# Performance work log

Hardware: AMD Instinct MI355X
Metric: run time of the kernel (lower is better)

The kernel has to match this reference:

```python
import jax, jax.numpy as jnp
import numpy as np

B, C, D, H, W = 2, 32, 96, 96, 96
RED = 16
INV_SQRT2 = 0.7071067811865476  # 1/sqrt(2), Haar analysis filter coefficient
BN_EPS = 1e-5


def _haar1(x, axis):
    # pywt 'haar' DWT on even-length signals: a[i]=(x[2i]+x[2i+1])/sqrt2, d[i]=(x[2i]-x[2i+1])/sqrt2
    e = jax.lax.slice_in_dim(x, 0, None, stride=2, axis=axis)
    o = jax.lax.slice_in_dim(x, 1, None, stride=2, axis=axis)
    return (e + o) * INV_SQRT2, (e - o) * INV_SQRT2


def haar_dwt3d(x):
    # x: (B, C, D, H, W). Separable 3D Haar DWT; key letters follow pywt dwtn
    # axis order (D, H, W): 'aad' = approx along D, approx along H, detail along W.
    aD, dD = _haar1(x, 2)
    aa, ad = _haar1(aD, 3)
    da, dd = _haar1(dD, 3)
    aaa, aad = _haar1(aa, 4)
    ada, add = _haar1(ad, 4)
    daa, dad = _haar1(da, 4)
    dda, ddd = _haar1(dd, 4)
    # per-channel grouping of 7 detail bands, then flatten to (B, 7C, D/2, H/2, W/2)
    high = jnp.stack([aad, ada, add, daa, dad, dda, ddd], axis=2)
    b, c = x.shape[0], x.shape[1]
    high = high.reshape(b, c * 7, *aaa.shape[2:])
    return aaa, high


def chan_attn(x, w1, w2):
    # AdaptiveAvgPool3d(1) -> FC(no bias) -> ReLU -> FC(no bias) -> Sigmoid -> scale
    y = x.mean(axis=(2, 3, 4))                     # (B, Ch)
    y = jax.nn.sigmoid(jnp.maximum(y @ w1.T, 0.0) @ w2.T)
    return x * y[:, :, None, None, None]


def setup_inputs() -> dict:
    key = jax.random.key(0)
    ks = jax.random.split(key, 7)
    x = jax.random.normal(ks[0], (B, C, D, H, W), dtype=jnp.float32)
    w1_low = jax.random.normal(ks[1], (C // RED, C), dtype=jnp.float32) * 0.1
    w2_low = jax.random.normal(ks[2], (C, C // RED), dtype=jnp.float32) * 0.1
    w1_high = jax.random.normal(ks[3], (7 * C // RED, 7 * C), dtype=jnp.float32) * 0.05
    w2_high = jax.random.normal(ks[4], (7 * C, 7 * C // RED), dtype=jnp.float32) * 0.05
    w_fuse = jax.random.normal(ks[5], (C, 8 * C), dtype=jnp.float32) * 0.05  # 1x1x1 conv kernel
    b_fuse = jnp.zeros((C,), dtype=jnp.float32)
    gamma = jnp.ones((C,), dtype=jnp.float32)
    beta = jnp.zeros((C,), dtype=jnp.float32)
    return dict(x=x, w1_low=w1_low, w2_low=w2_low, w1_high=w1_high, w2_high=w2_high,
                w_fuse=w_fuse, b_fuse=b_fuse, gamma=gamma, beta=beta)


def reference(x, w1_low, w2_low, w1_high, w2_high, w_fuse, b_fuse, gamma, beta):
    low, high = haar_dwt3d(x)                                  # (B,C,48,48,48), (B,7C,48,48,48)
    low = chan_attn(low, w1_low, w2_low)
    high = chan_attn(high, w1_high, w2_high)
    z = jnp.concatenate([low, high], axis=1)                   # (B, 8C, 48,48,48)
    z = jnp.einsum('bcdhw,oc->bodhw', z, w_fuse) + b_fuse[None, :, None, None, None]
    # BatchNorm3d (training-mode batch statistics, as fresh torch module defaults)
    mu = z.mean(axis=(0, 2, 3, 4), keepdims=True)
    var = z.var(axis=(0, 2, 3, 4), keepdims=True)
    z = (z - mu) * jax.lax.rsqrt(var + BN_EPS)
    z = z * gamma[None, :, None, None, None] + beta[None, :, None, None, None]
    return jnp.maximum(z, 0.0)
```

## Files before the change

kernel.cpp:

```cpp
#include <hip/hip_runtime.h>
#include <math.h>

#define HS 0.35355339059327373f
#define NSPAT 110592
#define NBN   221184

__global__ __launch_bounds__(256) void k1_parity(const float* __restrict__ x,
                                                 float* __restrict__ S) {
    int blk = blockIdx.x;
    int d   = blk % 96;
    int bc  = blk / 96;
    const float4* x4 = (const float4*)x + (long)blk * 2304;
    int tid = threadIdx.x;
    float aE0 = 0.f, aO0 = 0.f, aE1 = 0.f, aO1 = 0.f;
#pragma unroll
    for (int i = 0; i < 9; ++i) {
        int f = tid + i * 256;
        float4 v = x4[f];
        int h = f / 24;
        float e = v.x + v.z, o = v.y + v.w;
        if (h & 1) { aE1 += e; aO1 += o; }
        else       { aE0 += e; aO0 += o; }
    }
#pragma unroll
    for (int m = 32; m; m >>= 1) {
        aE0 += __shfl_xor(aE0, m, 64); aO0 += __shfl_xor(aO0, m, 64);
        aE1 += __shfl_xor(aE1, m, 64); aO1 += __shfl_xor(aO1, m, 64);
    }
    __shared__ float red[4][4];
    int lane = tid & 63, wave = tid >> 6;
    if (lane == 0) { red[wave][0] = aE0; red[wave][1] = aO0;
                     red[wave][2] = aE1; red[wave][3] = aO1; }
    __syncthreads();
    if (tid < 4) {
        float v = red[0][tid] + red[1][tid] + red[2][tid] + red[3][tid];
        int q = tid >> 1, r = tid & 1, p = d & 1;
        atomicAdd(&S[bc * 8 + p * 4 + q * 2 + r], v);
    }
}

__global__ __launch_bounds__(256) void k2_attn(
        const float* __restrict__ S,
        const float* __restrict__ w1l, const float* __restrict__ w2l,
        const float* __restrict__ w1h, const float* __restrict__ w2h,
        const float* __restrict__ wf, float* __restrict__ A) {
    int b = blockIdx.x >> 3, slice = blockIdx.x & 7;
    int tid = threadIdx.x;
    __shared__ float mlow[32], mhigh[224], h1l[2], h1h[14], ylow[32], yhigh[224];
    const float* Sb = S + b * 256;
    const float MS = HS / (float)NSPAT;

    {
        int c = tid >> 3, k = tid & 7;
        float s = 0.f;
        if (k == 0) {
#pragma unroll
            for (int j = 0; j < 8; ++j) s += Sb[c * 8 + j];
            mlow[c] = s * MS;
        } else {
#pragma unroll
            for (int j = 0; j < 8; ++j) {
                float sg = (__popc(j & k) & 1) ? -1.f : 1.f;
                s += sg * Sb[c * 8 + j];
            }
            mhigh[c * 7 + (k - 1)] = s * MS;
        }
    }
    __syncthreads();
    if (tid < 224) {
        int g = tid >> 4, l = tid & 15;
        float p = 0.f;
#pragma unroll
        for (int i = 0; i < 14; ++i)
            p += w1h[g * 224 + l * 14 + i] * mhigh[l * 14 + i];
#pragma unroll
        for (int m = 8; m; m >>= 1) p += __shfl_xor(p, m, 64);
        if (l == 0) h1h[g] = fmaxf(p, 0.f);
    } else {
        int j = (tid - 224) >> 4, l = tid & 15;
        float p = w1l[j * 32 + l] * mlow[l] + w1l[j * 32 + 16 + l] * mlow[16 + l];
#pragma unroll
        for (int m = 8; m; m >>= 1) p += __shfl_xor(p, m, 64);
        if (l == 0) h1l[j] = fmaxf(p, 0.f);
    }
    __syncthreads();
    if (tid < 32) {
        float s = w2l[tid * 2] * h1l[0] + w2l[tid * 2 + 1] * h1l[1];
        ylow[tid] = 1.f / (1.f + expf(-s));
    } else {
        int i = tid - 32;
        float s = 0.f;
#pragma unroll
        for (int j = 0; j < 14; ++j) s += w2h[i * 14 + j] * h1h[j];
        yhigh[i] = 1.f / (1.f + expf(-s));
    }
    __syncthreads();
#pragma unroll
    for (int it = 0; it < 4; ++it) {
        int idx = slice * 1024 + it * 256 + tid;
        int o = idx >> 8, c = (idx >> 3) & 31, pqr = idx & 7;
        float a = wf[o * 256 + c] * ylow[c];
#pragma unroll
        for (int k = 0; k < 7; ++k) {
            float sg = (__popc(pqr & (k + 1)) & 1) ? -1.f : 1.f;
            a += sg * wf[o * 256 + 32 + c * 7 + k] * yhigh[c * 7 + k];
        }
        A[b * 8192 + c * 256 + o * 8 + pqr] = a * HS;
    }
}

#define K3_LOAD(s, cc) { int i4_ = base + (cc) * 221184;                     \
    s##0 = x4[i4_]; s##1 = x4[i4_ + 24];                                     \
    s##2 = x4[i4_ + 2304]; s##3 = x4[i4_ + 2328]; }

#define K3_FMA(s, Aptr) {                                                    \
    _Pragma("unroll")                                                        \
    for (int o = 0; o < 16; ++o) {                                           \
        const float* Ao_ = (Aptr) + o * 8;        \
        float a0 = Ao_[0], a1 = Ao_[1], a2 = Ao_[2], a3 = Ao_[3];            \
        float a4 = Ao_[4], a5 = Ao_[5], a6 = Ao_[6], a7 = Ao_[7];            \
        acc0[o] += a0 * (s##0).x + a1 * (s##0).y + a2 * (s##1).x             \
                 + a3 * (s##1).y + a4 * (s##2).x + a5 * (s##2).y             \
                 + a6 * (s##3).x + a7 * (s##3).y;                            \
        acc1[o] += a0 * (s##0).z + a1 * (s##0).w + a2 * (s##1).z             \
                 + a3 * (s##1).w + a4 * (s##2).z + a5 * (s##2).w             \
                 + a6 * (s##3).z + a7 * (s##3).w;                            \
    } }

__global__ __launch_bounds__(192) void k3_main(const float* __restrict__ x,
                                               const float* __restrict__ A,
                                               float* __restrict__ z,
                                               float* __restrict__ bnSum,
                                               float* __restrict__ bnSq) {
    __shared__ float sA[4096];
    __shared__ float red[3][32];
    int blk  = blockIdx.x;
    int og   = (blk >> 3) & 1;
    int rest = (blk & 7) | ((blk >> 4) << 3);
    int ohg  = rest % 6;
    int tmp  = rest / 6;
    int od   = tmp % 48;
    int b    = tmp / 48;
    int tid = threadIdx.x;
    int row = tid / 24;
    int t   = tid % 24;
    int oh  = ohg * 8 + row;

    const float4* x4 = (const float4*)x;
    int base = (((b * 32) * 96 + 2 * od) * 96 + 2 * oh) * 24 + t;

    {
        const float4* A4 = (const float4*)A;
        int srcbase = b * 2048 + og * 32;
        float4* sA4 = (float4*)sA;
        for (int s = tid; s < 1024; s += 192) {
            int c = s >> 5, j = s & 31;
            sA4[s] = A4[srcbase + c * 64 + j];
        }
    }

    float acc0[16], acc1[16];
#pragma unroll
    for (int o = 0; o < 16; ++o) { acc0[o] = 0.f; acc1[o] = 0.f; }

    float4 pa0, pa1, pa2, pa3, pb0, pb1, pb2, pb3;
    K3_LOAD(pa, 0);
    __syncthreads();

    for (int c = 0; c < 32; c += 2) {
        K3_LOAD(pb, c + 1);
        const float* Ac = sA + c * 128;
        K3_FMA(pa, Ac);
        if (c + 2 < 32) K3_LOAD(pa, c + 2);
        K3_FMA(pb, Ac + 128);
    }

    float2* z2 = (float2*)z;
#pragma unroll
    for (int o = 0; o < 16; ++o) {
        int zi = (((b * 32 + og * 16 + o) * 48 + od) * 48 + oh) * 24 + t;
        z2[zi] = make_float2(acc0[o], acc1[o]);
    }

    int lane = tid & 63, wave = tid >> 6;
#pragma unroll
    for (int o = 0; o < 16; ++o) {
        float sv = acc0[o] + acc1[o];
        float qv = acc0[o] * acc0[o] + acc1[o] * acc1[o];
#pragma unroll
        for (int m = 32; m; m >>= 1) {
            sv += __shfl_xor(sv, m, 64);
            qv += __shfl_xor(qv, m, 64);
        }
        if (lane == 0) { red[wave][o] = sv; red[wave][16 + o] = qv; }
    }
    __syncthreads();
    if (tid < 32) {
        float v = red[0][tid] + red[1][tid] + red[2][tid];
        if (tid < 16) atomicAdd(&bnSum[og * 16 + tid], v);
        else          atomicAdd(&bnSq[og * 16 + tid - 16], v);
    }
}

__global__ __launch_bounds__(256) void k5_norm(float* __restrict__ z,
                                               const float* __restrict__ bnSum,
                                               const float* __restrict__ bnSq,
                                               const float* __restrict__ gamma,
                                               const float* __restrict__ beta) {
    __shared__ float s_sc[32], s_sh[32];
    int tid = threadIdx.x;
    if (tid < 32) {
        const float invN = 1.f / (float)NBN;
        float mean = bnSum[tid] * invN;
        float var  = bnSq[tid] * invN - mean * mean;
        float inv  = rsqrtf(var + 1e-5f);
        float sc   = gamma[tid] * inv;
        s_sc[tid] = sc;
        s_sh[tid] = beta[tid] - mean * sc;
    }
    int i = blockIdx.x * 256 + tid;
    float4* z4 = (float4*)z;
    float4 v = z4[i];
    __syncthreads();
    int o = (i / 27648) & 31;
    float sc = s_sc[o], sh = s_sh[o];
    v.x = fmaxf(v.x * sc + sh, 0.f);
    v.y = fmaxf(v.y * sc + sh, 0.f);
    v.z = fmaxf(v.z * sc + sh, 0.f);
    v.w = fmaxf(v.w * sc + sh, 0.f);
    z4[i] = v;
}

extern "C" void kernel_launch(void* const* d_in, const int* in_sizes, int n_in,
                              void* d_out, int out_size, void* d_ws, size_t ws_size,
                              hipStream_t stream) {
    const float* x    = (const float*)d_in[0];
    const float* w1l  = (const float*)d_in[1];
    const float* w2l  = (const float*)d_in[2];
    const float* w1h  = (const float*)d_in[3];
    const float* w2h  = (const float*)d_in[4];
    const float* wf   = (const float*)d_in[5];
    const float* gamma = (const float*)d_in[7];
    const float* beta  = (const float*)d_in[8];
    float* out = (float*)d_out;

    float* ws    = (float*)d_ws;
    float* S     = ws;
    float* bnSum = ws + 512;
    float* bnSq  = ws + 544;
    float* A     = ws + 1024;

    hipMemsetAsync(d_ws, 0, 576 * sizeof(float), stream);
    k1_parity<<<6144, 256, 0, stream>>>(x, S);
    k2_attn<<<16, 256, 0, stream>>>(S, w1l, w2l, w1h, w2h, wf, A);
    k3_main<<<1152, 192, 0, stream>>>(x, A, out, bnSum, bnSq);
    k5_norm<<<6912, 256, 0, stream>>>(out, bnSum, bnSq, gamma, beta);
}
```

Baseline: 439.9 us.

## Split k3 channel reduction across two thread halves with shared-memory combine

Doubles k3_main's block to 384 threads. Each half accumulates over 16 of the 32 input channels, and the second half's partial sums are added into the first half through a shared-memory buffer before the store and the BN statistics. The aim is more waves in flight to hide the global-load latency of the streaming x reads. The cost is an extra 12KB of LDS, extra barriers and an exchange step.

Result: slower. 923.7 us (+110.0%).

```diff
diff --git a/kernel.cpp b/kernel.cpp
--- a/kernel.cpp
+++ b/kernel.cpp
@@ -113,10 +113,10 @@
     s##0 = x4[i4_]; s##1 = x4[i4_ + 24];                                     \
     s##2 = x4[i4_ + 2304]; s##3 = x4[i4_ + 2328]; }
 
-#define K3_FMA(s, Aptr) {                                                    \
+#define K3_FMA(s, Ac) {                                                      \
     _Pragma("unroll")                                                        \
     for (int o = 0; o < 16; ++o) {                                           \
-        const float* Ao_ = (Aptr) + o * 8;        \
+        const float* Ao_ = (Ac) + o * 8;          \
         float a0 = Ao_[0], a1 = Ao_[1], a2 = Ao_[2], a3 = Ao_[3];            \
         float a4 = Ao_[4], a5 = Ao_[5], a6 = Ao_[6], a7 = Ao_[7];            \
         acc0[o] += a0 * (s##0).x + a1 * (s##0).y + a2 * (s##1).x             \
@@ -127,12 +127,13 @@
                  + a6 * (s##3).z + a7 * (s##3).w;                            \
     } }
 
-__global__ __launch_bounds__(192) void k3_main(const float* __restrict__ x,
-                                               const float* __restrict__ A,
-                                               float* __restrict__ z,
-                                               float* __restrict__ bnSum,
-                                               float* __restrict__ bnSq) {
+__global__ __launch_bounds__(384, 4) void k3_main(const float* __restrict__ x,
+                                                  const float* __restrict__ A,
+                                                  float* __restrict__ z,
+                                                  float* __restrict__ bnSum,
+                                                  float* __restrict__ bnSq) {
     __shared__ float sA[4096];
+    __shared__ float redbuf[16][192];
     __shared__ float red[3][32];
     int blk  = blockIdx.x;
     int og   = (blk >> 3) & 1;
@@ -141,10 +142,13 @@
     int tmp  = rest / 6;
     int od   = tmp % 48;
     int b    = tmp / 48;
-    int tid = threadIdx.x;
-    int row = tid / 24;
-    int t   = tid % 24;
+    int tid   = threadIdx.x;
+    int kpart = tid / 192;
+    int tl    = tid % 192;
+    int row = tl / 24;
+    int t   = tl % 24;
     int oh  = ohg * 8 + row;
+    int cbase = kpart * 16;
 
     const float4* x4 = (const float4*)x;
     int base = (((b * 32) * 96 + 2 * od) * 96 + 2 * oh) * 24 + t;
@@ -153,7 +157,7 @@
         const float4* A4 = (const float4*)A;
         int srcbase = b * 2048 + og * 32;
         float4* sA4 = (float4*)sA;
-        for (int s = tid; s < 1024; s += 192) {
+        for (int s = tid; s < 1024; s += 384) {
             int c = s >> 5, j = s & 31;
             sA4[s] = A4[srcbase + c * 64 + j];
         }
@@ -164,35 +168,56 @@
     for (int o = 0; o < 16; ++o) { acc0[o] = 0.f; acc1[o] = 0.f; }
 
     float4 pa0, pa1, pa2, pa3, pb0, pb1, pb2, pb3;
-    K3_LOAD(pa, 0);
-    __syncthreads();
-
-    for (int c = 0; c < 32; c += 2) {
-        K3_LOAD(pb, c + 1);
-        const float* Ac = sA + c * 128;
+    K3_LOAD(pa, cbase);
+    __syncthreads();
+
+    for (int c = 0; c < 16; c += 2) {
+        K3_LOAD(pb, cbase + c + 1);
+        const float* Ac = sA + (cbase + c) * 128;
         K3_FMA(pa, Ac);
-        if (c + 2 < 32) K3_LOAD(pa, c + 2);
+        if (c + 2 < 16) K3_LOAD(pa, cbase + c + 2);
         K3_FMA(pb, Ac + 128);
     }
 
-    float2* z2 = (float2*)z;
-#pragma unroll
-    for (int o = 0; o < 16; ++o) {
-        int zi = (((b * 32 + og * 16 + o) * 48 + od) * 48 + oh) * 24 + t;
-        z2[zi] = make_float2(acc0[o], acc1[o]);
-    }
-
-    int lane = tid & 63, wave = tid >> 6;
-#pragma unroll
-    for (int o = 0; o < 16; ++o) {
-        float sv = acc0[o] + acc1[o];
-        float qv = acc0[o] * acc0[o] + acc1[o] * acc1[o];
-#pragma unroll
-        for (int m = 32; m; m >>= 1) {
-            sv += __shfl_xor(sv, m, 64);
-            qv += __shfl_xor(qv, m, 64);
-        }
-        if (lane == 0) { red[wave][o] = sv; red[wave][16 + o] = qv; }
+#pragma unroll
+    for (int j = 0; j < 2; ++j) {
+        if (kpart == 1) {
+#pragma unroll
+            for (int i = 0; i < 8; ++i) {
+                redbuf[2 * i][tl]     = acc0[8 * j + i];
+                redbuf[2 * i + 1][tl] = acc1[8 * j + i];
+            }
+        }
+        __syncthreads();
+        if (kpart == 0) {
+#pragma unroll
+            for (int i = 0; i < 8; ++i) {
+                acc0[8 * j + i] += redbuf[2 * i][tl];
+                acc1[8 * j + i] += redbuf[2 * i + 1][tl];
+            }
+        }
+        __syncthreads();
+    }
+
+    if (kpart == 0) {
+        float2* z2 = (float2*)z;
+#pragma unroll
+        for (int o = 0; o < 16; ++o) {
+            int zi = (((b * 32 + og * 16 + o) * 48 + od) * 48 + oh) * 24 + t;
+            z2[zi] = make_float2(acc0[o], acc1[o]);
+        }
+        int lane = tid & 63, wave = tid >> 6;
+#pragma unroll
+        for (int o = 0; o < 16; ++o) {
+            float sv = acc0[o] + acc1[o];
+            float qv = acc0[o] * acc0[o] + acc1[o] * acc1[o];
+#pragma unroll
+            for (int m = 32; m; m >>= 1) {
+                sv += __shfl_xor(sv, m, 64);
+                qv += __shfl_xor(qv, m, 64);
+            }
+            if (lane == 0) { red[wave][o] = sv; red[wave][16 + o] = qv; }
+        }
     }
     __syncthreads();
     if (tid < 32) {
@@ -253,6 +278,6 @@
     hipMemsetAsync(d_ws, 0, 576 * sizeof(float), stream);
     k1_parity<<<6144, 256, 0, stream>>>(x, S);
     k2_attn<<<16, 256, 0, stream>>>(S, w1l, w2l, w1h, w2h, wf, A);
-    k3_main<<<1152, 192, 0, stream>>>(x, A, out, bnSum, bnSq);
+    k3_main<<<1152, 384, 0, stream>>>(x, A, out, bnSum, bnSq);
     k5_norm<<<6912, 256, 0, stream>>>(out, bnSum, bnSq, gamma, beta);
 }
```

## Split k3 output channels across two thread groups per block

Applied to the files above, without the earlier changes.

Doubles k3_main block size to 384 threads, with each 192-thread half computing 8 of the 16 output channels for the same spatial tile. Per-thread accumulators drop from 32 to 16 and the manual double-buffered prefetch of x is replaced by a simple per-channel load loop. This lowers register pressure to raise occupancy and latency hiding, but each x element is now loaded by two thread groups, doubling global/L2 read traffic for the input, and the explicit software prefetch is gone.

Result: no change. 436.1 us (-0.9%).

```diff
diff --git a/kernel.cpp b/kernel.cpp
--- a/kernel.cpp
+++ b/kernel.cpp
@@ -109,31 +109,13 @@
     }
 }
 
-#define K3_LOAD(s, cc) { int i4_ = base + (cc) * 221184;                     \
-    s##0 = x4[i4_]; s##1 = x4[i4_ + 24];                                     \
-    s##2 = x4[i4_ + 2304]; s##3 = x4[i4_ + 2328]; }
-
-#define K3_FMA(s, Aptr) {                                                    \
-    _Pragma("unroll")                                                        \
-    for (int o = 0; o < 16; ++o) {                                           \
-        const float* Ao_ = (Aptr) + o * 8;        \
-        float a0 = Ao_[0], a1 = Ao_[1], a2 = Ao_[2], a3 = Ao_[3];            \
-        float a4 = Ao_[4], a5 = Ao_[5], a6 = Ao_[6], a7 = Ao_[7];            \
-        acc0[o] += a0 * (s##0).x + a1 * (s##0).y + a2 * (s##1).x             \
-                 + a3 * (s##1).y + a4 * (s##2).x + a5 * (s##2).y             \
-                 + a6 * (s##3).x + a7 * (s##3).y;                            \
-        acc1[o] += a0 * (s##0).z + a1 * (s##0).w + a2 * (s##1).z             \
-                 + a3 * (s##1).w + a4 * (s##2).z + a5 * (s##2).w             \
-                 + a6 * (s##3).z + a7 * (s##3).w;                            \
-    } }
-
-__global__ __launch_bounds__(192) void k3_main(const float* __restrict__ x,
+__global__ __launch_bounds__(384) void k3_main(const float* __restrict__ x,
                                                const float* __restrict__ A,
                                                float* __restrict__ z,
                                                float* __restrict__ bnSum,
                                                float* __restrict__ bnSq) {
     __shared__ float sA[4096];
-    __shared__ float red[3][32];
+    __shared__ float red[6][16];
     int blk  = blockIdx.x;
     int og   = (blk >> 3) & 1;
     int rest = (blk & 7) | ((blk >> 4) << 3);
@@ -141,9 +123,11 @@
     int tmp  = rest / 6;
     int od   = tmp % 48;
     int b    = tmp / 48;
-    int tid = threadIdx.x;
-    int row = tid / 24;
-    int t   = tid % 24;
+    int tid  = threadIdx.x;
+    int ogrp = tid / 192;
+    int tl   = tid % 192;
+    int row = tl / 24;
+    int t   = tl % 24;
     int oh  = ohg * 8 + row;
 
     const float4* x4 = (const float4*)x;
@@ -153,38 +137,50 @@
         const float4* A4 = (const float4*)A;
         int srcbase = b * 2048 + og * 32;
         float4* sA4 = (float4*)sA;
-        for (int s = tid; s < 1024; s += 192) {
+        for (int s = tid; s < 1024; s += 384) {
             int c = s >> 5, j = s & 31;
             sA4[s] = A4[srcbase + c * 64 + j];
         }
     }
 
-    float acc0[16], acc1[16];
-#pragma unroll
-    for (int o = 0; o < 16; ++o) { acc0[o] = 0.f; acc1[o] = 0.f; }
-
-    float4 pa0, pa1, pa2, pa3, pb0, pb1, pb2, pb3;
-    K3_LOAD(pa, 0);
-    __syncthreads();
-
-    for (int c = 0; c < 32; c += 2) {
-        K3_LOAD(pb, c + 1);
-        const float* Ac = sA + c * 128;
-        K3_FMA(pa, Ac);
-        if (c + 2 < 32) K3_LOAD(pa, c + 2);
-        K3_FMA(pb, Ac + 128);
+    float acc0[8], acc1[8];
+#pragma unroll
+    for (int o = 0; o < 8; ++o) { acc0[o] = 0.f; acc1[o] = 0.f; }
+
+    __syncthreads();
+
+    const float* Acg = sA + ogrp * 64;
+#pragma unroll 1
+    for (int c = 0; c < 32; ++c) {
+        int i4 = base + c * 221184;
+        float4 v00 = x4[i4];
+        float4 v01 = x4[i4 + 24];
+        float4 v10 = x4[i4 + 2304];
+        float4 v11 = x4[i4 + 2328];
+        const float* Ac = Acg + c * 128;
+#pragma unroll
+        for (int o = 0; o < 8; ++o) {
+            const float* Ao = Ac + o * 8;
+            float a0 = Ao[0], a1 = Ao[1], a2 = Ao[2], a3 = Ao[3];
+            float a4 = Ao[4], a5 = Ao[5], a6 = Ao[6], a7 = Ao[7];
+            acc0[o] += a0 * v00.x + a1 * v00.y + a2 * v01.x + a3 * v01.y
+                     + a4 * v10.x + a5 * v10.y + a6 * v11.x + a7 * v11.y;
+            acc1[o] += a0 * v00.z + a1 * v00.w + a2 * v01.z + a3 * v01.w
+                     + a4 * v10.z + a5 * v10.w + a6 * v11.z + a7 * v11.w;
+        }
     }
 
     float2* z2 = (float2*)z;
 #pragma unroll
-    for (int o = 0; o < 16; ++o) {
-        int zi = (((b * 32 + og * 16 + o) * 48 + od) * 48 + oh) * 24 + t;
+    for (int o = 0; o < 8; ++o) {
+        int och = og * 16 + ogrp * 8 + o;
+        int zi = (((b * 32 + och) * 48 + od) * 48 + oh) * 24 + t;
         z2[zi] = make_float2(acc0[o], acc1[o]);
     }
 
     int lane = tid & 63, wave = tid >> 6;
 #pragma unroll
-    for (int o = 0; o < 16; ++o) {
+    for (int o = 0; o < 8; ++o) {
         float sv = acc0[o] + acc1[o];
         float qv = acc0[o] * acc0[o] + acc1[o] * acc1[o];
 #pragma unroll
@@ -192,13 +188,18 @@
             sv += __shfl_xor(sv, m, 64);
             qv += __shfl_xor(qv, m, 64);
         }
-        if (lane == 0) { red[wave][o] = sv; red[wave][16 + o] = qv; }
+        if (lane == 0) { red[wave][o] = sv; red[wave][8 + o] = qv; }
     }
     __syncthreads();
     if (tid < 32) {
-        float v = red[0][tid] + red[1][tid] + red[2][tid];
-        if (tid < 16) atomicAdd(&bnSum[og * 16 + tid], v);
-        else          atomicAdd(&bnSq[og * 16 + tid - 16], v);
+        int i   = tid & 7;
+        int grp = (tid >> 3) & 1;
+        int w0  = grp * 3;
+        int off = (tid < 16) ? 0 : 8;
+        float v = red[w0][off + i] + red[w0 + 1][off + i] + red[w0 + 2][off + i];
+        int ch = og * 16 + grp * 8 + i;
+        if (tid < 16) atomicAdd(&bnSum[ch], v);
+        else          atomicAdd(&bnSq[ch], v);
     }
 }
 
@@ -253,6 +254,6 @@
     hipMemsetAsync(d_ws, 0, 576 * sizeof(float), stream);
     k1_parity<<<6144, 256, 0, stream>>>(x, S);
     k2_attn<<<16, 256, 0, stream>>>(S, w1l, w2l, w1h, w2h, wf, A);
-    k3_main<<<1152, 192, 0, stream>>>(x, A, out, bnSum, bnSq);
+    k3_main<<<1152, 384, 0, stream>>>(x, A, out, bnSum, bnSq);
     k5_norm<<<6912, 256, 0, stream>>>(out, bnSum, bnSq, gamma, beta);
 }
```
